# Kernel tuning notes

Measured on AMD Instinct MI355X. Metric: run time of the kernel, lower is better.

Reference implementation:

```python
import jax, jax.numpy as jnp
import numpy as np

# Conv hyperparams (from init_kwargs)
STRIDE = (1, 1)
PADDING = (1, 1)
DILATION = (1, 1)

AQMIN, AQMAX = 0.0, 15.0   # uint4 activation range
WQMIN, WQMAX = -8.0, 7.0   # int4 weight range


def setup_inputs() -> dict:
    key = jax.random.key(0)
    k1, k2 = jax.random.split(key)
    # Activations in [0, 16) so uint4 quantization is non-trivial
    x = jax.random.uniform(k1, (32, 64, 112, 112), dtype=jnp.float32) * 16.0
    # Weights spread over int4 range
    w = jax.random.normal(k2, (128, 64, 3, 3), dtype=jnp.float32) * 4.0
    return {"x": x, "w": w}


def reference(x, w):
    # Quantize: activations -> uint4 [0,15], weights -> int4 [-8,7]
    q_in = jnp.clip(jnp.round(x), AQMIN, AQMAX)
    q_w = jnp.clip(jnp.round(w), WQMIN, WQMAX)
    # im2col unfold + matmul in the original == standard convolution.
    # Integer-valued fp32 math is exact here (|acc| << 2^24).
    out = jax.lax.conv_general_dilated(
        q_in, q_w,
        window_strides=STRIDE,
        padding=[(PADDING[0], PADDING[0]), (PADDING[1], PADDING[1])],
        rhs_dilation=DILATION,
        dimension_numbers=("NCHW", "OIHW", "NCHW"),
    )
    return out.astype(jnp.float32)  # [32, 128, 112, 112]
```

## Files before the change

### kernel.cpp

```cpp
#include <hip/hip_runtime.h>


#define CIN  64
#define HH   112
#define WW   112
#define HW   (HH * WW)
#define COUT 128
#define KTOT 576
#define HP   114
#define WP   114
#define WHALF 36864

#define XQ_BYTES (32 * HP * WP * 64)
#define NWBLK 288
#define NXBLK (32 * 57)
#define NCONV 1568

typedef __attribute__((ext_vector_type(4))) int int32x4;

__global__ __launch_bounds__(256) void k_prep(const float* __restrict__ x,
                                              const float* __restrict__ w,
                                              char* __restrict__ xq,
                                              char* __restrict__ wq) {
    const int bid = blockIdx.x, tid = threadIdx.x;
    if (bid < NWBLK) {
        int idx = bid * 256 + tid;
        int h   = idx / WHALF;
        int r1  = idx % WHALF;
        int ks  = r1 / 4096;
        int r2  = r1 % 4096;
        int tO  = r2 / 1024;
        int r3  = r2 % 1024;
        int ln  = r3 / 16;
        int j   = r3 % 16;
        int o   = h * 64 + tO * 16 + (ln & 15);
        int c   = (ln >> 4) * 16 + j;
        int kh  = ks / 3, kw = ks % 3;
        float q = fminf(fmaxf(rintf(w[((o * CIN + c) * 3 + kh) * 3 + kw]), -8.0f), 7.0f);
        wq[idx] = (char)(int)q;
        return;
    }
    const int rid = bid - NWBLK;
    const int n  = rid / 57;
    const int hp = (rid % 57) * 2 + (tid >> 7);
    const int wp = tid & 127;
    if (wp >= WP) return;
    char* dst = xq + (((size_t)n * HP + hp) * WP + wp) * 64;
    int32x4* d4 = (int32x4*)dst;
    if (hp == 0 || hp == HP - 1 || wp == 0 || wp == WP - 1) {
#pragma unroll
        for (int i = 0; i < 4; ++i) d4[i] = (int32x4)(0);
        return;
    }
    const int h = hp - 1, ww = wp - 1;
    const float* px = x + (((size_t)n * CIN) * HH + h) * WW + ww;
    unsigned int buf[16];
#pragma unroll
    for (int cw = 0; cw < 16; ++cw) {
        unsigned int word = 0;
#pragma unroll
        for (int j = 0; j < 4; ++j) {
            float v = px[(size_t)(cw * 4 + j) * HW];
            float q = fminf(fmaxf(rintf(v), 0.0f), 15.0f);
            word |= ((unsigned int)(int)q) << (8 * j);
        }
        buf[cw] = word;
    }
#pragma unroll
    for (int i = 0; i < 4; ++i) {
        int32x4 v;
        v.x = (int)buf[i * 4 + 0];
        v.y = (int)buf[i * 4 + 1];
        v.z = (int)buf[i * 4 + 2];
        v.w = (int)buf[i * 4 + 3];
        d4[i] = v;
    }
}

__global__ __launch_bounds__(256) void k_conv(const char* __restrict__ xq,
                                              const char* __restrict__ wq,
                                              float* __restrict__ out) {
    __shared__ char wlds[WHALF];

    const int tid = threadIdx.x;
    const int nid  = (blockIdx.x & 7) * (NCONV / 8) + (blockIdx.x >> 3);
    const int half = nid & 1;
    const int pb   = nid >> 1;

    const char* wsrc = wq + (size_t)half * WHALF;
    for (int i = tid; i < WHALF / 16; i += 256)
        *(int32x4*)(&wlds[i * 16]) = *(const int32x4*)(wsrc + i * 16);
    __syncthreads();

    const int wave = tid >> 6;
    const int lane = tid & 63;
    const int l15  = lane & 15;
    const int lk   = lane >> 4;

#pragma unroll
    for (int it = 0; it < 2; ++it) {
        const int chunk = pb * 2 + it;
        const int n  = chunk / 49;
        const int s0 = (chunk % 49) * 256 + wave * 64;
        const char* xbase = xq + (size_t)n * (HP * WP * 64);

        int saddr[4];
#pragma unroll
        for (int tS = 0; tS < 4; ++tS) {
            int sl = s0 + tS * 16 + l15;
            int hh = sl / WW;
            int ww = sl - hh * WW;
            saddr[tS] = (hh * WP + ww) * 64 + lk * 16;
        }

        int32x4 acc[4][4];
#pragma unroll
        for (int i = 0; i < 4; ++i)
#pragma unroll
            for (int j = 0; j < 4; ++j) acc[i][j] = (int32x4)(0);

        int32x4 af[4], afn[4];
#pragma unroll
        for (int tS = 0; tS < 4; ++tS)
            af[tS] = *(const int32x4*)(xbase + saddr[tS]);

#pragma unroll
        for (int ks = 0; ks < 9; ++ks) {
            if (ks < 8) {
                const int ksn = ks + 1;
                const int koffn = ((ksn / 3) * WP + (ksn % 3)) * 64;
#pragma unroll
                for (int tS = 0; tS < 4; ++tS)
                    afn[tS] = *(const int32x4*)(xbase + saddr[tS] + koffn);
            }
#pragma unroll
            for (int tO = 0; tO < 4; ++tO) {
                const int32x4 bf = *(const int32x4*)(
                    &wlds[(ks * 4 + tO) * 1024 + lane * 16]);
#pragma unroll
                for (int tS = 0; tS < 4; ++tS)
                    acc[tS][tO] = __builtin_amdgcn_mfma_i32_16x16x64_i8(af[tS], bf, acc[tS][tO], 0, 0, 0);
            }
#pragma unroll
            for (int tS = 0; tS < 4; ++tS) af[tS] = afn[tS];
        }

        float* obase = out + (size_t)n * (COUT * HW) + (size_t)half * 64 * HW;
#pragma unroll
        for (int tS = 0; tS < 4; ++tS) {
#pragma unroll
            for (int tO = 0; tO < 4; ++tO) {
                const int co = tO * 16 + l15;
                const int sl = s0 + tS * 16 + lk * 4;
                float4 v;
                v.x = (float)acc[tS][tO][0];
                v.y = (float)acc[tS][tO][1];
                v.z = (float)acc[tS][tO][2];
                v.w = (float)acc[tS][tO][3];
                *(float4*)(&obase[(size_t)co * HW + sl]) = v;
            }
        }
    }
}

extern "C" void kernel_launch(void* const* d_in, const int* in_sizes, int n_in,
                              void* d_out, int out_size, void* d_ws, size_t ws_size,
                              hipStream_t stream) {
    const float* x = (const float*)d_in[0];
    const float* w = (const float*)d_in[1];
    float* out = (float*)d_out;

    char* xq = (char*)d_ws;
    char* wq = xq + XQ_BYTES;

    hipLaunchKernelGGL(k_prep, dim3(NWBLK + NXBLK), dim3(256), 0, stream, x, w, xq, wq);
    hipLaunchKernelGGL(k_conv, dim3(NCONV), dim3(256), 0, stream, xq, wq, out);
}
```

Measured before the change: 105.4 us.

## Stage activation row slab in LDS and stream weights from global

The conv kernel is restructured so each 512-thread block handles two output rows of one image across all 128 output channels. It stages a 4-row padded activation slab in shared memory and reads weights directly from global/L2, with a one-step register prefetch. The weight layout in the prep kernel changes to match this, dropping the two-halves split of output channels. This is meant to cut the redundant global activation reads across the 9 taps and the per-block 36KB weight LDS fill. In exchange every block fetches weights from global memory, and LDS bank conflicts may appear on the slab reads.

```diff
diff --git a/kernel.cpp b/kernel.cpp
--- a/kernel.cpp
+++ b/kernel.cpp
@@ -6,15 +6,17 @@
 #define WW   112
 #define HW   (HH * WW)
 #define COUT 128
-#define KTOT 576
 #define HP   114
 #define WP   114
-#define WHALF 36864
+#define KTOT 576
 
 #define XQ_BYTES (32 * HP * WP * 64)
 #define NWBLK 288
 #define NXBLK (32 * 57)
-#define NCONV 1568
+#define NCONV 1792
+
+#define SLAB_BYTES (4 * WP * 64)
+#define SLAB_U16   (SLAB_BYTES / 16)
 
 typedef __attribute__((ext_vector_type(4))) int int32x4;
 
@@ -25,15 +27,13 @@
     const int bid = blockIdx.x, tid = threadIdx.x;
     if (bid < NWBLK) {
         int idx = bid * 256 + tid;
-        int h   = idx / WHALF;
-        int r1  = idx % WHALF;
-        int ks  = r1 / 4096;
-        int r2  = r1 % 4096;
-        int tO  = r2 / 1024;
+        int ks  = idx / 8192;
+        int r2  = idx % 8192;
+        int ct  = r2 / 1024;
         int r3  = r2 % 1024;
         int ln  = r3 / 16;
         int j   = r3 % 16;
-        int o   = h * 64 + tO * 16 + (ln & 15);
+        int o   = ct * 16 + (ln & 15);
         int c   = (ln >> 4) * 16 + j;
         int kh  = ks / 3, kw = ks % 3;
         float q = fminf(fmaxf(rintf(w[((o * CIN + c) * 3 + kh) * 3 + kw]), -8.0f), 7.0f);
@@ -77,88 +77,78 @@
     }
 }
 
-__global__ __launch_bounds__(256) void k_conv(const char* __restrict__ xq,
-                                              const char* __restrict__ wq,
-                                              float* __restrict__ out) {
-    __shared__ char wlds[WHALF];
+__global__ __launch_bounds__(512, 4) void k_conv(const char* __restrict__ xq,
+                                                 const char* __restrict__ wq,
+                                                 float* __restrict__ out) {
+    __shared__ char slab[SLAB_BYTES];
 
     const int tid = threadIdx.x;
-    const int nid  = (blockIdx.x & 7) * (NCONV / 8) + (blockIdx.x >> 3);
-    const int half = nid & 1;
-    const int pb   = nid >> 1;
+    const int nid = (blockIdx.x & 7) * (NCONV / 8) + (blockIdx.x >> 3);
+    const int n   = nid / 56;
+    const int h0  = (nid % 56) * 2;
 
-    const char* wsrc = wq + (size_t)half * WHALF;
-    for (int i = tid; i < WHALF / 16; i += 256)
-        *(int32x4*)(&wlds[i * 16]) = *(const int32x4*)(wsrc + i * 16);
+    const char* src = xq + (size_t)n * (HP * WP * 64) + (size_t)h0 * (WP * 64);
+#pragma unroll
+    for (int k = 0; k < 4; ++k) {
+        const int u = tid + k * 512;
+        if (u < SLAB_U16)
+            *(int32x4*)(&slab[u * 16]) = *(const int32x4*)(src + u * 16);
+    }
     __syncthreads();
 
     const int wave = tid >> 6;
     const int lane = tid & 63;
     const int l15  = lane & 15;
     const int lk   = lane >> 4;
+    const int rw   = wave >> 2;
+    const int Q    = wave & 3;
+
+    const char* wbase = wq + (Q * 2) * 1024 + lane * 16;
+
+    int32x4 acc[7][2];
+#pragma unroll
+    for (int i = 0; i < 7; ++i) {
+        acc[i][0] = (int32x4)(0);
+        acc[i][1] = (int32x4)(0);
+    }
+
+    int32x4 bf[2], bfn[2];
+    bf[0] = *(const int32x4*)(wbase);
+    bf[1] = *(const int32x4*)(wbase + 1024);
 
 #pragma unroll
-    for (int it = 0; it < 2; ++it) {
-        const int chunk = pb * 2 + it;
-        const int n  = chunk / 49;
-        const int s0 = (chunk % 49) * 256 + wave * 64;
-        const char* xbase = xq + (size_t)n * (HP * WP * 64);
+    for (int ks = 0; ks < 9; ++ks) {
+        if (ks < 8) {
+            bfn[0] = *(const int32x4*)(wbase + (ks + 1) * 8192);
+            bfn[1] = *(const int32x4*)(wbase + (ks + 1) * 8192 + 1024);
+        }
+        const int kh = ks / 3, kw = ks % 3;
+        const char* arow = &slab[(((rw + kh) * WP) + l15 + kw) * 64 + lk * 16];
+        int32x4 af[7];
+#pragma unroll
+        for (int wt = 0; wt < 7; ++wt)
+            af[wt] = *(const int32x4*)(arow + wt * 1024);
+#pragma unroll
+        for (int tO = 0; tO < 2; ++tO)
+#pragma unroll
+            for (int wt = 0; wt < 7; ++wt)
+                acc[wt][tO] = __builtin_amdgcn_mfma_i32_16x16x64_i8(af[wt], bf[tO], acc[wt][tO], 0, 0, 0);
+        bf[0] = bfn[0];
+        bf[1] = bfn[1];
+    }
 
-        int saddr[4];
+    const int hgl = h0 + rw;
 #pragma unroll
-        for (int tS = 0; tS < 4; ++tS) {
-            int sl = s0 + tS * 16 + l15;
-            int hh = sl / WW;
-            int ww = sl - hh * WW;
-            saddr[tS] = (hh * WP + ww) * 64 + lk * 16;
-        }
-
-        int32x4 acc[4][4];
+    for (int wt = 0; wt < 7; ++wt) {
 #pragma unroll
-        for (int i = 0; i < 4; ++i)
-#pragma unroll
-            for (int j = 0; j < 4; ++j) acc[i][j] = (int32x4)(0);
-
-        int32x4 af[4], afn[4];
-#pragma unroll
-        for (int tS = 0; tS < 4; ++tS)
-            af[tS] = *(const int32x4*)(xbase + saddr[tS]);
-
-#pragma unroll
-        for (int ks = 0; ks < 9; ++ks) {
-            if (ks < 8) {
-                const int ksn = ks + 1;
-                const int koffn = ((ksn / 3) * WP + (ksn % 3)) * 64;
-#pragma unroll
-                for (int tS = 0; tS < 4; ++tS)
-                    afn[tS] = *(const int32x4*)(xbase + saddr[tS] + koffn);
-            }
-#pragma unroll
-            for (int tO = 0; tO < 4; ++tO) {
-                const int32x4 bf = *(const int32x4*)(
-                    &wlds[(ks * 4 + tO) * 1024 + lane * 16]);
-#pragma unroll
-                for (int tS = 0; tS < 4; ++tS)
-                    acc[tS][tO] = __builtin_amdgcn_mfma_i32_16x16x64_i8(af[tS], bf, acc[tS][tO], 0, 0, 0);
-            }
-#pragma unroll
-            for (int tS = 0; tS < 4; ++tS) af[tS] = afn[tS];
-        }
-
-        float* obase = out + (size_t)n * (COUT * HW) + (size_t)half * 64 * HW;
-#pragma unroll
-        for (int tS = 0; tS < 4; ++tS) {
-#pragma unroll
-            for (int tO = 0; tO < 4; ++tO) {
-                const int co = tO * 16 + l15;
-                const int sl = s0 + tS * 16 + lk * 4;
-                float4 v;
-                v.x = (float)acc[tS][tO][0];
-                v.y = (float)acc[tS][tO][1];
-                v.z = (float)acc[tS][tO][2];
-                v.w = (float)acc[tS][tO][3];
-                *(float4*)(&obase[(size_t)co * HW + sl]) = v;
-            }
+        for (int tO = 0; tO < 2; ++tO) {
+            const int co = Q * 32 + tO * 16 + l15;
+            float4 v;
+            v.x = (float)acc[wt][tO][0];
+            v.y = (float)acc[wt][tO][1];
+            v.z = (float)acc[wt][tO][2];
+            v.w = (float)acc[wt][tO][3];
+            *(float4*)(&out[(((size_t)n * COUT + co) * HH + hgl) * WW + wt * 16 + lk * 4]) = v;
         }
     }
 }
@@ -174,5 +164,5 @@
     char* wq = xq + XQ_BYTES;
 
     hipLaunchKernelGGL(k_prep, dim3(NWBLK + NXBLK), dim3(256), 0, stream, x, w, xq, wq);
-    hipLaunchKernelGGL(k_conv, dim3(NCONV), dim3(256), 0, stream, xq, wq, out);
+    hipLaunchKernelGGL(k_conv, dim3(NCONV), dim3(512), 0, stream, xq, wq, out);
 }
```

Measured after the change: 90.62 us. 1.16x faster.
